# Optimization experiments

Hardware: AMD Instinct MI355X
Metric: run time of the kernel (lower is better)

Reference implementation:

```python
import jax, jax.numpy as jnp
import numpy as np

N = 100000

def _gcn_norm(edge_index, n):
    row, col = edge_index[0], edge_index[1]
    deg = jnp.zeros((n,), jnp.float32).at[col].add(1.0)
    dinv = jnp.where(deg > 0, jax.lax.rsqrt(jnp.maximum(deg, 1.0)), 0.0)
    return dinv[row] * dinv[col]


def _arma_conv(x, row, col, norm, init_w, w, root_w, bias):
    # x: [N, Fin]; init_w: [K, Fin, F]; w: [T-1, K, F, F]; root_w: [T, K, Fin, F]; bias: [T, K, 1, F]
    out = jnp.einsum('nf,kfg->kng', x, init_w)  # [K, N, F]
    T = root_w.shape[0]
    for t in range(T):
        if t > 0:
            out = jnp.einsum('kng,kgh->knh', out, w[t - 1])
        msg = out[:, row, :] * norm[None, :, None]          # [K, E, F] gather
        out = jnp.zeros_like(out).at[:, col, :].add(msg)    # scatter-add to targets
        out = out + jnp.einsum('nf,kfg->kng', x, root_w[t]) + bias[t]
        out = jax.nn.relu(out)
    return out.mean(axis=0)  # average over stacks K


def setup_inputs() -> dict:
    key = jax.random.key(0)
    ks = jax.random.split(key, 12)
    E, Fin, H, C, K = 1600000, 128, 64, 41, 2
    s = 0.1
    return {
        'x': jax.random.normal(ks[0], (N, Fin), jnp.float32),
        'edge_index': jax.random.randint(ks[1], (2, E), 0, N, jnp.int64),
        'w1_init': jax.random.normal(ks[2], (K, Fin, H), jnp.float32) * s,
        'w1': jax.random.normal(ks[3], (1, K, H, H), jnp.float32) * s,
        'w1_root': jax.random.normal(ks[4], (2, K, Fin, H), jnp.float32) * s,
        'b1': jax.random.normal(ks[5], (2, K, 1, H), jnp.float32) * s,
        'w2_init': jax.random.normal(ks[6], (K, H, C), jnp.float32) * s,
        'w2': jax.random.normal(ks[7], (1, K, C, C), jnp.float32) * s,
        'w2_root': jax.random.normal(ks[8], (2, K, H, C), jnp.float32) * s,
        'b2': jax.random.normal(ks[9], (2, K, 1, C), jnp.float32) * s,
    }


def reference(x, edge_index, w1_init, w1, w1_root, b1, w2_init, w2, w2_root, b2):
    row, col = edge_index[0], edge_index[1]
    norm = _gcn_norm(edge_index, N)
    h = jax.nn.relu(_arma_conv(x, row, col, norm, w1_init, w1, w1_root, b1))
    # F.dropout is identity in eval mode
    h = _arma_conv(h, row, col, norm, w2_init, w2, w2_root, b2)
    return jax.nn.log_softmax(h, axis=1)
```

## Files before the change

### kernel.cpp

```cpp
#include <hip/hip_runtime.h>
#include <math.h>

#define TPB 256
typedef unsigned short ushort_t;
typedef unsigned int uint_t;
typedef __attribute__((ext_vector_type(8))) short bf16x8;
typedef __attribute__((ext_vector_type(4))) float f32x4;

__device__ __forceinline__ float bf2f(ushort_t h) {
    return __uint_as_float(((uint_t)h) << 16);
}
__device__ __forceinline__ ushort_t f2bf(float f) {
    uint_t u = __float_as_uint(f);
    u += 0x7fff + ((u >> 16) & 1);
    return (ushort_t)(u >> 16);
}
__device__ __forceinline__ uint_t pack2(float x, float y) {
    return (uint_t)f2bf(x) | ((uint_t)f2bf(y) << 16);
}

__global__ void rank_kernel(const int* __restrict__ col, int* __restrict__ cnt,
                            unsigned short* __restrict__ pos, int E) {
    int e = blockIdx.x * blockDim.x + threadIdx.x;
    if (e < E) pos[e] = (unsigned short)atomicAdd(&cnt[col[e]], 1);
}

__global__ void scan_block(const int* __restrict__ cnt, int* __restrict__ incl,
                           int* __restrict__ bsum, int N) {
    __shared__ int s[TPB];
    int i = blockIdx.x * TPB + threadIdx.x;
    s[threadIdx.x] = (i < N) ? ((cnt[i] + 3) & ~3) : 0;
    __syncthreads();
    for (int d = 1; d < TPB; d <<= 1) {
        int t = (threadIdx.x >= d) ? s[threadIdx.x - d] : 0;
        __syncthreads();
        s[threadIdx.x] += t;
        __syncthreads();
    }
    if (i < N) incl[i] = s[threadIdx.x];
    if (threadIdx.x == TPB - 1) bsum[blockIdx.x] = s[TPB - 1];
}

__global__ void scan_bsums(int* __restrict__ bsum, int nb) {
    __shared__ int s[512];
    int t = threadIdx.x;
    int v = (t < nb) ? bsum[t] : 0;
    s[t] = v;
    __syncthreads();
    for (int d = 1; d < 512; d <<= 1) {
        int u = (t >= d) ? s[t - d] : 0;
        __syncthreads();
        s[t] += u;
        __syncthreads();
    }
    if (t < nb) bsum[t] = s[t] - v;
}

__global__ void finalize_csr(const int* __restrict__ incl, const int* __restrict__ bsum,
                             const int* __restrict__ cnt, int* __restrict__ rowstart,
                             float* __restrict__ dinv, int N) {
    int i = blockIdx.x * TPB + threadIdx.x;
    if (i < N) {
        rowstart[i + 1] = incl[i] + bsum[blockIdx.x];
        int d = cnt[i];
        dinv[i] = (d > 0) ? rsqrtf((float)d) : 0.0f;
    }
    if (i == 0) rowstart[0] = 0;
}

__global__ void fill_csr(const int* __restrict__ row, const int* __restrict__ col,
                         const int* __restrict__ rowstart, const unsigned short* __restrict__ pos,
                         int* __restrict__ srcidx, int E) {
    int e = blockIdx.x * blockDim.x + threadIdx.x;
    if (e < E) srcidx[rowstart[col[e]] + (int)pos[e]] = row[e];
}

__global__ void pad_csr(const int* __restrict__ rowstart, const int* __restrict__ cnt,
                        int* __restrict__ srcidx, int N) {
    int i = blockIdx.x * blockDim.x + threadIdx.x;
    if (i >= N) return;
    int b = rowstart[i] + cnt[i], en = rowstart[i + 1];
    for (int e = b; e < en; ++e) srcidx[e] = N;
}

__global__ void cvt4_kernel(const float4* __restrict__ src, uint2* __restrict__ dst, int n4) {
    int i = blockIdx.x * blockDim.x + threadIdx.x;
    if (i < n4) {
        float4 v = src[i];
        dst[i] = make_uint2(pack2(v.x, v.y), pack2(v.z, v.w));
    }
}

#define SWZ_A 32768
#define SWZ_B 24576
#define SWZ_C 12288
#define SWZ_D 12288
__global__ void swz_all(const float* __restrict__ w1_init, const float* __restrict__ w1,
                        const float* __restrict__ w1_root, const float* __restrict__ w2_init,
                        const float* __restrict__ w2, const float* __restrict__ w2_root,
                        short* __restrict__ dst) {
    int idx = blockIdx.x * blockDim.x + threadIdx.x;
    int region, base, CH, CT;
    if (idx < SWZ_A)                          { region = 0; base = 0; CH = 4; CT = 8; }
    else if (idx < SWZ_A + SWZ_B)             { region = 1; base = SWZ_A; CH = 6; CT = 4; }
    else if (idx < SWZ_A + SWZ_B + SWZ_C)     { region = 2; base = SWZ_A + SWZ_B; CH = 2; CT = 6; }
    else if (idx < SWZ_A + SWZ_B + SWZ_C + SWZ_D)
                                              { region = 3; base = SWZ_A + SWZ_B + SWZ_C; CH = 4; CT = 3; }
    else return;
    int r = idx - base;
    int j = r & 7, ln = (r >> 3) & 63;
    int rest = r >> 9;
    int ct = rest % CT, c = (rest / CT) % CH, k = rest / (CT * CH);
    int col = ct * 16 + (ln & 15);
    int kl = (ln >> 4) * 8 + j;
    float v = 0.0f;
    if (region == 0) {
        int kk = c * 32 + kl;
        if (col < 64)       v = w1_init[((size_t)k * 128 + kk) * 64 + col];
        else                v = w1_root[((size_t)k * 128 + kk) * 64 + (col - 64)];
    } else if (region == 1) {
        if (c < 2) { int kk = c * 32 + kl;        v = w1[((size_t)k * 64 + kk) * 64 + col]; }
        else       { int kk = (c - 2) * 32 + kl;  v = w1_root[((size_t)(2 + k) * 128 + kk) * 64 + col]; }
    } else if (region == 2) {
        int kk = c * 32 + kl;
        if (col < 48) { if (col < 41)            v = w2_init[((size_t)k * 64 + kk) * 41 + col]; }
        else          { int c2 = col - 48; if (c2 < 41) v = w2_root[((size_t)k * 64 + kk) * 41 + c2]; }
    } else {
        if (c < 2) { int kk = c * 32 + kl;       if (kk < 41 && col < 41) v = w2[((size_t)k * 41 + kk) * 41 + col]; }
        else       { int kk = (c - 2) * 32 + kl; if (col < 41)            v = w2_root[((size_t)(2 + k) * 64 + kk) * 41 + col]; }
    }
    dst[(size_t)base + r] = (short)f2bf(v);
}

template<int CT, int CTA, int CH>
__global__ __launch_bounds__(256, 4)
void gemm_t0(const ushort_t* __restrict__ s2, int s2s, const short* __restrict__ fragbuf,
             const float* __restrict__ biasB, const float* __restrict__ dinv,
             int FB, int N, uint_t* __restrict__ pre, uint_t* __restrict__ outH) {
    constexpr int PP = (CT - CTA) * 8;
    constexpr int PA = CTA * 8;
    const int k = blockIdx.y;
    const int n0 = blockIdx.x * 128;
    const int t = threadIdx.x;
    const int w = t >> 6, lane = t & 63, quad = lane >> 4, lr = lane & 15;
    const short* fb = fragbuf + (size_t)k * CH * CT * 512;

    int r0 = n0 + w * 32 + lr;
    int m0 = r0 < N ? r0 : N - 1;
    int m1 = (r0 + 16) < N ? (r0 + 16) : N - 1;

    bf16x8 a0v[CH], a1v[CH];
#pragma unroll
    for (int c = 0; c < CH; ++c) {
        int off = c * 32 + quad * 8;
        a0v[c] = *(const bf16x8*)&s2[(size_t)m0 * s2s + off];
        a1v[c] = *(const bf16x8*)&s2[(size_t)m1 * s2s + off];
    }

    __shared__ short lds_b[CH * CT * 512];
    {
        constexpr int CHUNKS = CH * CT * 64;
#pragma unroll
        for (int i = 0; i < (CHUNKS + 255) / 256; ++i) {
            int idx = i * 256 + t;
            if (CHUNKS % 256 == 0 || idx < CHUNKS)
                *(bf16x8*)&lds_b[idx * 8] = *(const bf16x8*)&fb[(size_t)idx * 8];
        }
    }
    __syncthreads();

    f32x4 acc[2][CT];
#pragma unroll
    for (int rt = 0; rt < 2; ++rt)
#pragma unroll
        for (int ct = 0; ct < CT; ++ct) acc[rt][ct] = (f32x4){0.f, 0.f, 0.f, 0.f};

#pragma unroll
    for (int c = 0; c < CH; ++c) {
#pragma unroll
        for (int ct = 0; ct < CT; ++ct) {
            bf16x8 b = *(const bf16x8*)&lds_b[((size_t)c * CT + ct) * 512 + lane * 8];
            acc[0][ct] = __builtin_amdgcn_mfma_f32_16x16x32_bf16(a0v[c], b, acc[0][ct], 0, 0, 0);
            acc[1][ct] = __builtin_amdgcn_mfma_f32_16x16x32_bf16(a1v[c], b, acc[1][ct], 0, 0, 0);
        }
    }

#pragma unroll
    for (int rt = 0; rt < 2; ++rt) {
#pragma unroll
        for (int i = 0; i < 4; ++i) {
            int n = n0 + w * 32 + rt * 16 + quad * 4 + i;
            if (n >= N) continue;
            float dnv = dinv[n];
#pragma unroll
            for (int ct = 0; ct < CT; ++ct) {
                int col = ct * 16 + lr;
                float v = acc[rt][ct][i];
                if (ct < CTA) {
                    v *= dnv;
                } else {
                    int c2 = col - CTA * 16;
                    if (c2 < FB) v += biasB[(size_t)k * FB + c2];
                }
                float vn = __shfl_xor(v, 1);
                uint_t p = pack2(v, vn);
                uint_t p2 = __shfl_xor(p, 2);
                if (!(lr & 3)) {
                    if (ct < CTA) {
                        *(uint2*)&outH[((size_t)n * 2 + k) * PA + (col >> 1)] = make_uint2(p, p2);
                    } else {
                        int c2 = col - CTA * 16;
                        *(uint2*)&pre[((size_t)n * 2 + k) * PP + (c2 >> 1)] = make_uint2(p, p2);
                    }
                }
            }
        }
    }
}

__global__ __launch_bounds__(256, 3)
void gemm_t1_l1(const ushort_t* __restrict__ s1, const ushort_t* __restrict__ xh,
                const short* __restrict__ fragbuf, const float* __restrict__ bias,
                int N, uint_t* __restrict__ hhU) {
    constexpr int CT = 4, CH = 6;
    const int n0 = blockIdx.x * 128;
    const int t = threadIdx.x;
    const int w = t >> 6, lane = t & 63, quad = lane >> 4, lr = lane & 15;

    int r0 = n0 + w * 32 + lr;
    int m0 = r0 < N ? r0 : N - 1;
    int m1 = (r0 + 16) < N ? (r0 + 16) : N - 1;

    bf16x8 s0a[2][2], s1a[2][2];
    bf16x8 x0a[4], x1a[4];
#pragma unroll
    for (int c = 0; c < 2; ++c) {
        int off = c * 32 + quad * 8;
#pragma unroll
        for (int kk = 0; kk < 2; ++kk) {
            s0a[c][kk] = *(const bf16x8*)&s1[((size_t)m0 * 2 + kk) * 64 + off];
            s1a[c][kk] = *(const bf16x8*)&s1[((size_t)m1 * 2 + kk) * 64 + off];
        }
    }
#pragma unroll
    for (int c = 0; c < 4; ++c) {
        int off = c * 32 + quad * 8;
        x0a[c] = *(const bf16x8*)&xh[(size_t)m0 * 128 + off];
        x1a[c] = *(const bf16x8*)&xh[(size_t)m1 * 128 + off];
    }

    __shared__ short lds_b[2 * CH * CT * 512];
    {
        constexpr int CHUNKS = 2 * CH * CT * 64;
#pragma unroll
        for (int i = 0; i < CHUNKS / 256; ++i) {
            int idx = i * 256 + t;
            *(bf16x8*)&lds_b[idx * 8] = *(const bf16x8*)&fragbuf[(size_t)idx * 8];
        }
    }
    __syncthreads();

    f32x4 acc[2][2][CT];
#pragma unroll
    for (int k = 0; k < 2; ++k)
#pragma unroll
        for (int rt = 0; rt < 2; ++rt)
#pragma unroll
            for (int ct = 0; ct < CT; ++ct) acc[k][rt][ct] = (f32x4){0.f, 0.f, 0.f, 0.f};

#pragma unroll
    for (int c = 0; c < CH; ++c) {
#pragma unroll
        for (int k = 0; k < 2; ++k) {
            bf16x8 a0 = (c < 2) ? s0a[c][k] : x0a[c - 2];
            bf16x8 a1 = (c < 2) ? s1a[c][k] : x1a[c - 2];
#pragma unroll
            for (int ct = 0; ct < CT; ++ct) {
                bf16x8 b = *(const bf16x8*)&lds_b[(((size_t)k * CH + c) * CT + ct) * 512 + lane * 8];
                acc[k][0][ct] = __builtin_amdgcn_mfma_f32_16x16x32_bf16(a0, b, acc[k][0][ct], 0, 0, 0);
                acc[k][1][ct] = __builtin_amdgcn_mfma_f32_16x16x32_bf16(a1, b, acc[k][1][ct], 0, 0, 0);
            }
        }
    }

#pragma unroll
    for (int rt = 0; rt < 2; ++rt) {
#pragma unroll
        for (int i = 0; i < 4; ++i) {
            int n = n0 + w * 32 + rt * 16 + quad * 4 + i;
            if (n >= N) continue;
#pragma unroll
            for (int ct = 0; ct < CT; ++ct) {
                int col = ct * 16 + lr;
                float v0 = fmaxf(acc[0][rt][ct][i] + bias[col], 0.0f);
                float v1 = fmaxf(acc[1][rt][ct][i] + bias[64 + col], 0.0f);
                float m = 0.5f * (v0 + v1);
                float mn = __shfl_xor(m, 1);
                uint_t p = pack2(m, mn);
                uint_t p2 = __shfl_xor(p, 2);
                if (!(lr & 3)) *(uint2*)&hhU[(size_t)n * 32 + (col >> 1)] = make_uint2(p, p2);
            }
        }
    }
}

__global__ __launch_bounds__(256, 3)
void gemm_t1_l2(const ushort_t* __restrict__ s1, const ushort_t* __restrict__ hh,
                const short* __restrict__ fragbuf, const float* __restrict__ bias,
                int N, float* __restrict__ out) {
    constexpr int CT = 3, CH = 4;
    const int n0 = blockIdx.x * 128;
    const int t = threadIdx.x;
    const int w = t >> 6, lane = t & 63, quad = lane >> 4, lr = lane & 15;

    int r0 = n0 + w * 32 + lr;
    int m0 = r0 < N ? r0 : N - 1;
    int m1 = (r0 + 16) < N ? (r0 + 16) : N - 1;

    bf16x8 s0a[2][2], s1a[2][2];
    bf16x8 h0a[2], h1a[2];
#pragma unroll
    for (int c = 0; c < 2; ++c) {
        int off = c * 32 + quad * 8;
#pragma unroll
        for (int kk = 0; kk < 2; ++kk) {
            s0a[c][kk] = *(const bf16x8*)&s1[((size_t)m0 * 2 + kk) * 48 + off];
            s1a[c][kk] = *(const bf16x8*)&s1[((size_t)m1 * 2 + kk) * 48 + off];
        }
    }
#pragma unroll
    for (int c = 0; c < 2; ++c) {
        int off = c * 32 + quad * 8;
        h0a[c] = *(const bf16x8*)&hh[(size_t)m0 * 64 + off];
        h1a[c] = *(const bf16x8*)&hh[(size_t)m1 * 64 + off];
    }

    __shared__ short lds_b[2 * CH * CT * 512];
    {
        constexpr int CHUNKS = 2 * CH * CT * 64;
#pragma unroll
        for (int i = 0; i < CHUNKS / 256; ++i) {
            int idx = i * 256 + t;
            *(bf16x8*)&lds_b[idx * 8] = *(const bf16x8*)&fragbuf[(size_t)idx * 8];
        }
    }
    __syncthreads();

    f32x4 acc[2][2][CT];
#pragma unroll
    for (int k = 0; k < 2; ++k)
#pragma unroll
        for (int rt = 0; rt < 2; ++rt)
#pragma unroll
            for (int ct = 0; ct < CT; ++ct) acc[k][rt][ct] = (f32x4){0.f, 0.f, 0.f, 0.f};

#pragma unroll
    for (int c = 0; c < CH; ++c) {
#pragma unroll
        for (int k = 0; k < 2; ++k) {
            bf16x8 a0 = (c < 2) ? s0a[c][k] : h0a[c - 2];
            bf16x8 a1 = (c < 2) ? s1a[c][k] : h1a[c - 2];
#pragma unroll
            for (int ct = 0; ct < CT; ++ct) {
                bf16x8 b = *(const bf16x8*)&lds_b[(((size_t)k * CH + c) * CT + ct) * 512 + lane * 8];
                acc[k][0][ct] = __builtin_amdgcn_mfma_f32_16x16x32_bf16(a0, b, acc[k][0][ct], 0, 0, 0);
                acc[k][1][ct] = __builtin_amdgcn_mfma_f32_16x16x32_bf16(a1, b, acc[k][1][ct], 0, 0, 0);
            }
        }
    }

#pragma unroll
    for (int rt = 0; rt < 2; ++rt) {
#pragma unroll
        for (int i = 0; i < 4; ++i) {
            int n = n0 + w * 32 + rt * 16 + quad * 4 + i;
            float m[CT];
            float mx = -1e30f;
#pragma unroll
            for (int ct = 0; ct < CT; ++ct) {
                int col = ct * 16 + lr;
                float b0 = (col < 41) ? bias[col] : 0.0f;
                float b1v = (col < 41) ? bias[41 + col] : 0.0f;
                float v0 = fmaxf(acc[0][rt][ct][i] + b0, 0.0f);
                float v1 = fmaxf(acc[1][rt][ct][i] + b1v, 0.0f);
                m[ct] = 0.5f * (v0 + v1);
                if (col < 41) mx = fmaxf(mx, m[ct]);
            }
#pragma unroll
            for (int msk = 1; msk < 16; msk <<= 1) mx = fmaxf(mx, __shfl_xor(mx, msk));
            float s = 0.0f;
#pragma unroll
            for (int ct = 0; ct < CT; ++ct) {
                int col = ct * 16 + lr;
                if (col < 41) s += __expf(m[ct] - mx);
            }
#pragma unroll
            for (int msk = 1; msk < 16; msk <<= 1) s += __shfl_xor(s, msk);
            float ls = __logf(s);
            if (n < N) {
#pragma unroll
                for (int ct = 0; ct < CT; ++ct) {
                    int col = ct * 16 + lr;
                    if (col < 41) out[(size_t)n * 41 + col] = m[ct] - mx - ls;
                }
            }
        }
    }
}

template<int PAIRS, bool SCALE_OUT>
__global__ __launch_bounds__(256)
void gather(const int* __restrict__ rowstart, const int* __restrict__ srcidx,
            const float* __restrict__ dinv, const uint_t* __restrict__ msg,
            const uint_t* __restrict__ pre, uint_t* __restrict__ outH, int N) {
    int gt = blockIdx.x * 256 + threadIdx.x;
    int n = gt >> 6, lane = gt & 63;
    if (n >= N) return;
    int k, pair;
    if (PAIRS == 32) { k = lane >> 5; pair = lane & 31; }
    else { k = lane / PAIRS; pair = lane - k * PAIRS; }
    if (k >= 2) return;
    const int STR = 2 * PAIRS;
    const uint_t lo = (uint_t)(k * PAIRS + pair);
    int beg = rowstart[n], end = rowstart[n + 1];
    float dn = dinv[n];
    size_t o = (size_t)n * STR + lo;
    uint_t p = 0;
    if (pre) p = pre[o];

    float ax0 = 0.f, ax1 = 0.f, ay0 = 0.f, ay1 = 0.f;
    int e = beg;
    for (; e + 8 <= end; e += 8) {
        int4 sa = *(const int4*)&srcidx[e];
        int4 sb = *(const int4*)&srcidx[e + 4];
        uint_t m0 = msg[(uint_t)(sa.x * STR) + lo];
        uint_t m1 = msg[(uint_t)(sa.y * STR) + lo];
        uint_t m2 = msg[(uint_t)(sa.z * STR) + lo];
        uint_t m3 = msg[(uint_t)(sa.w * STR) + lo];
        uint_t m4 = msg[(uint_t)(sb.x * STR) + lo];
        uint_t m5 = msg[(uint_t)(sb.y * STR) + lo];
        uint_t m6 = msg[(uint_t)(sb.z * STR) + lo];
        uint_t m7 = msg[(uint_t)(sb.w * STR) + lo];
        ax0 += __uint_as_float(m0 << 16); ay0 += __uint_as_float(m0 & 0xffff0000u);
        ax1 += __uint_as_float(m1 << 16); ay1 += __uint_as_float(m1 & 0xffff0000u);
        ax0 += __uint_as_float(m2 << 16); ay0 += __uint_as_float(m2 & 0xffff0000u);
        ax1 += __uint_as_float(m3 << 16); ay1 += __uint_as_float(m3 & 0xffff0000u);
        ax0 += __uint_as_float(m4 << 16); ay0 += __uint_as_float(m4 & 0xffff0000u);
        ax1 += __uint_as_float(m5 << 16); ay1 += __uint_as_float(m5 & 0xffff0000u);
        ax0 += __uint_as_float(m6 << 16); ay0 += __uint_as_float(m6 & 0xffff0000u);
        ax1 += __uint_as_float(m7 << 16); ay1 += __uint_as_float(m7 & 0xffff0000u);
    }
    if (e < end) {
        int4 sa = *(const int4*)&srcidx[e];
        uint_t m0 = msg[(uint_t)(sa.x * STR) + lo];
        uint_t m1 = msg[(uint_t)(sa.y * STR) + lo];
        uint_t m2 = msg[(uint_t)(sa.z * STR) + lo];
        uint_t m3 = msg[(uint_t)(sa.w * STR) + lo];
        ax0 += __uint_as_float(m0 << 16); ay0 += __uint_as_float(m0 & 0xffff0000u);
        ax1 += __uint_as_float(m1 << 16); ay1 += __uint_as_float(m1 & 0xffff0000u);
        ax0 += __uint_as_float(m2 << 16); ay0 += __uint_as_float(m2 & 0xffff0000u);
        ax1 += __uint_as_float(m3 << 16); ay1 += __uint_as_float(m3 & 0xffff0000u);
    }
    float ax = (ax0 + ax1) * dn;
    float ay = (ay0 + ay1) * dn;
    if (pre) {
        ax = fmaxf(ax + bf2f((ushort_t)p), 0.0f);
        ay = fmaxf(ay + bf2f((ushort_t)(p >> 16)), 0.0f);
    }
    if (SCALE_OUT) { ax *= dn; ay *= dn; }
    outH[o] = pack2(ax, ay);
}

extern "C" void kernel_launch(void* const* d_in, const int* in_sizes, int n_in,
                              void* d_out, int out_size, void* d_ws, size_t ws_size,
                              hipStream_t stream) {
    const float* x       = (const float*)d_in[0];
    const int*   ei      = (const int*)  d_in[1];
    const float* w1_init = (const float*)d_in[2];
    const float* w1      = (const float*)d_in[3];
    const float* w1_root = (const float*)d_in[4];
    const float* b1      = (const float*)d_in[5];
    const float* w2_init = (const float*)d_in[6];
    const float* w2      = (const float*)d_in[7];
    const float* w2_root = (const float*)d_in[8];
    const float* b2      = (const float*)d_in[9];

    const int Fin1 = 128;
    int N = in_sizes[0] / Fin1;
    int E = in_sizes[1] / 2;
    const int* row = ei;
    const int* col = ei + E;

    char* ws = (char*)d_ws;
    size_t off = 0;
    auto carve = [&](size_t bytes) -> void* {
        void* p = ws + off;
        off += (bytes + 255) & ~(size_t)255;
        return p;
    };
    int nblkN = (N + TPB - 1) / TPB;
    int*      cnt      = (int*)     carve((size_t)N * 4);
    int*      incl     = (int*)     carve((size_t)N * 4);
    int*      rowstart = (int*)     carve((size_t)(N + 1) * 4);
    int*      bsum     = (int*)     carve((size_t)nblkN * 4);
    float*    dinv     = (float*)   carve((size_t)N * 4);
    unsigned short* pos = (unsigned short*)carve((size_t)E * 2);
    int*      srcidx   = (int*)     carve((size_t)(E + 3 * (size_t)N + 64) * 4);
    short*    swz      = (short*)   carve((size_t)(SWZ_A + SWZ_B + SWZ_C + SWZ_D) * 2);
    ushort_t* xh       = (ushort_t*)carve((size_t)N * 128 * 2);
    ushort_t* hh       = (ushort_t*)carve((size_t)N * 64 * 2);
    ushort_t* b16A     = (ushort_t*)carve((size_t)N * 2 * 64 * 2 + 256);
    ushort_t* b16B     = (ushort_t*)carve((size_t)N * 2 * 64 * 2 + 256);
    uint_t*   pre      = (uint_t*)  carve((size_t)N * 2 * 32 * 4);

    hipMemsetAsync((char*)b16A + (size_t)N * 256, 0, 256, stream);
    hipMemsetAsync((char*)b16B + (size_t)N * 256, 0, 256, stream);

    hipMemsetAsync(cnt, 0, (size_t)N * 4, stream);
    rank_kernel <<<(E + TPB - 1) / TPB, TPB, 0, stream>>>(col, cnt, pos, E);
    scan_block  <<<nblkN, TPB, 0, stream>>>(cnt, incl, bsum, N);
    scan_bsums  <<<1, 512, 0, stream>>>(bsum, nblkN);
    finalize_csr<<<nblkN, TPB, 0, stream>>>(incl, bsum, cnt, rowstart, dinv, N);
    pad_csr     <<<nblkN, TPB, 0, stream>>>(rowstart, cnt, srcidx, N);
    fill_csr    <<<(E + TPB - 1) / TPB, TPB, 0, stream>>>(row, col, rowstart, pos, srcidx, E);

    int swztot = SWZ_A + SWZ_B + SWZ_C + SWZ_D;
    swz_all<<<(swztot + TPB - 1) / TPB, TPB, 0, stream>>>(w1_init, w1, w1_root,
                                                          w2_init, w2, w2_root, swz);
    int nx4 = N * 128 / 4;
    cvt4_kernel<<<(nx4 + TPB - 1) / TPB, TPB, 0, stream>>>((const float4*)x, (uint2*)xh, nx4);

    dim3 gg2((N + 127) / 128, 2);
    dim3 gg1((N + 127) / 128, 1);
    int ggb = (N * 64 + TPB - 1) / TPB;
    const short* swzA = swz;
    const short* swzB = swz + SWZ_A;
    const short* swzC = swz + SWZ_A + SWZ_B;
    const short* swzD = swz + SWZ_A + SWZ_B + SWZ_C;

    gemm_t0<8, 4, 4><<<gg2, TPB, 0, stream>>>(xh, 128, swzA, b1, dinv, 64, N, pre, (uint_t*)b16A);
    gather<32, true ><<<ggb, TPB, 0, stream>>>(rowstart, srcidx, dinv, (const uint_t*)b16A,
                                               pre, (uint_t*)b16B, N);
    gather<32, false><<<ggb, TPB, 0, stream>>>(rowstart, srcidx, dinv, (const uint_t*)b16B,
                                               nullptr, (uint_t*)b16A, N);
    gemm_t1_l1<<<gg1, TPB, 0, stream>>>(b16A, xh, swzB, b1 + 2 * 64, N, (uint_t*)hh);

    hipMemsetAsync((char*)b16A + (size_t)N * 192, 0, 192, stream);
    hipMemsetAsync((char*)b16B + (size_t)N * 192, 0, 192, stream);

    gemm_t0<6, 3, 2><<<gg2, TPB, 0, stream>>>(hh, 64, swzC, b2, dinv, 41, N, pre, (uint_t*)b16A);
    gather<24, true ><<<ggb, TPB, 0, stream>>>(rowstart, srcidx, dinv, (const uint_t*)b16A,
                                               pre, (uint_t*)b16B, N);
    gather<24, false><<<ggb, TPB, 0, stream>>>(rowstart, srcidx, dinv, (const uint_t*)b16B,
                                               nullptr, (uint_t*)b16A, N);
    gemm_t1_l2<<<gg1, TPB, 0, stream>>>(b16A, hh, swzD, b2 + 2 * 41, N, (float*)d_out);
}
```

Baseline: 563.0 us.

## Fuse preprocessing kernels, overlap CSR fill with first GEMM, tighten layer-2 gather

Merges the edge-rank, weight-swizzle and x-to-bf16 conversion into one launch, since those three steps are independent. Folds the CSR fill and pad work into extra blocks of the first GEMM, interleaved so both run concurrently. Specialises the layer-2 gather to use 48 threads per node instead of 64, which removes idle lanes. This cuts launch count and tail idle time, but the fused GEMM grid now has mixed block types that may hurt occupancy or LDS scheduling.

Result: slower. 592.2 us (+5.2%).

```diff
diff --git a/kernel.cpp b/kernel.cpp
--- a/kernel.cpp
+++ b/kernel.cpp
@@ -19,10 +19,64 @@
     return (uint_t)f2bf(x) | ((uint_t)f2bf(y) << 16);
 }
 
-__global__ void rank_kernel(const int* __restrict__ col, int* __restrict__ cnt,
-                            unsigned short* __restrict__ pos, int E) {
-    int e = blockIdx.x * blockDim.x + threadIdx.x;
-    if (e < E) pos[e] = (unsigned short)atomicAdd(&cnt[col[e]], 1);
+#define SWZ_A 32768
+#define SWZ_B 24576
+#define SWZ_C 12288
+#define SWZ_D 12288
+
+__global__ __launch_bounds__(256)
+void pre1(const int* __restrict__ col, int* __restrict__ cnt, unsigned short* __restrict__ pos,
+          int E, int nEb,
+          const float* __restrict__ w1_init, const float* __restrict__ w1,
+          const float* __restrict__ w1_root, const float* __restrict__ w2_init,
+          const float* __restrict__ w2, const float* __restrict__ w2_root,
+          short* __restrict__ swzdst, int nSb,
+          const float4* __restrict__ x, uint2* __restrict__ xh, int n4) {
+    int b = blockIdx.x;
+    if (b < nEb) {
+        int e = b * 256 + threadIdx.x;
+        if (e < E) pos[e] = (unsigned short)atomicAdd(&cnt[col[e]], 1);
+        return;
+    }
+    if (b < nEb + nSb) {
+        int idx = (b - nEb) * 256 + threadIdx.x;
+        int region, base, CH, CT;
+        if (idx < SWZ_A)                          { region = 0; base = 0; CH = 4; CT = 8; }
+        else if (idx < SWZ_A + SWZ_B)             { region = 1; base = SWZ_A; CH = 6; CT = 4; }
+        else if (idx < SWZ_A + SWZ_B + SWZ_C)     { region = 2; base = SWZ_A + SWZ_B; CH = 2; CT = 6; }
+        else if (idx < SWZ_A + SWZ_B + SWZ_C + SWZ_D)
+                                                  { region = 3; base = SWZ_A + SWZ_B + SWZ_C; CH = 4; CT = 3; }
+        else return;
+        int r = idx - base;
+        int j = r & 7, ln = (r >> 3) & 63;
+        int rest = r >> 9;
+        int ct = rest % CT, c = (rest / CT) % CH, k = rest / (CT * CH);
+        int colm = ct * 16 + (ln & 15);
+        int kl = (ln >> 4) * 8 + j;
+        float v = 0.0f;
+        if (region == 0) {
+            int kk = c * 32 + kl;
+            if (colm < 64)       v = w1_init[((size_t)k * 128 + kk) * 64 + colm];
+            else                 v = w1_root[((size_t)k * 128 + kk) * 64 + (colm - 64)];
+        } else if (region == 1) {
+            if (c < 2) { int kk = c * 32 + kl;        v = w1[((size_t)k * 64 + kk) * 64 + colm]; }
+            else       { int kk = (c - 2) * 32 + kl;  v = w1_root[((size_t)(2 + k) * 128 + kk) * 64 + colm]; }
+        } else if (region == 2) {
+            int kk = c * 32 + kl;
+            if (colm < 48) { if (colm < 41)           v = w2_init[((size_t)k * 64 + kk) * 41 + colm]; }
+            else           { int c2 = colm - 48; if (c2 < 41) v = w2_root[((size_t)k * 64 + kk) * 41 + c2]; }
+        } else {
+            if (c < 2) { int kk = c * 32 + kl;       if (kk < 41 && colm < 41) v = w2[((size_t)k * 41 + kk) * 41 + colm]; }
+            else       { int kk = (c - 2) * 32 + kl; if (colm < 41)            v = w2_root[((size_t)(2 + k) * 64 + kk) * 41 + colm]; }
+        }
+        swzdst[(size_t)base + r] = (short)f2bf(v);
+        return;
+    }
+    int i = (b - nEb - nSb) * 256 + threadIdx.x;
+    if (i < n4) {
+        float4 v = x[i];
+        xh[i] = make_uint2(pack2(v.x, v.y), pack2(v.z, v.w));
+    }
 }
 
 __global__ void scan_block(const int* __restrict__ cnt, int* __restrict__ incl,
@@ -68,79 +122,47 @@
     if (i == 0) rowstart[0] = 0;
 }
 
-__global__ void fill_csr(const int* __restrict__ row, const int* __restrict__ col,
-                         const int* __restrict__ rowstart, const unsigned short* __restrict__ pos,
-                         int* __restrict__ srcidx, int E) {
-    int e = blockIdx.x * blockDim.x + threadIdx.x;
-    if (e < E) srcidx[rowstart[col[e]] + (int)pos[e]] = row[e];
-}
-
-__global__ void pad_csr(const int* __restrict__ rowstart, const int* __restrict__ cnt,
-                        int* __restrict__ srcidx, int N) {
-    int i = blockIdx.x * blockDim.x + threadIdx.x;
-    if (i >= N) return;
-    int b = rowstart[i] + cnt[i], en = rowstart[i + 1];
-    for (int e = b; e < en; ++e) srcidx[e] = N;
-}
-
-__global__ void cvt4_kernel(const float4* __restrict__ src, uint2* __restrict__ dst, int n4) {
-    int i = blockIdx.x * blockDim.x + threadIdx.x;
-    if (i < n4) {
-        float4 v = src[i];
-        dst[i] = make_uint2(pack2(v.x, v.y), pack2(v.z, v.w));
-    }
-}
-
-#define SWZ_A 32768
-#define SWZ_B 24576
-#define SWZ_C 12288
-#define SWZ_D 12288
-__global__ void swz_all(const float* __restrict__ w1_init, const float* __restrict__ w1,
-                        const float* __restrict__ w1_root, const float* __restrict__ w2_init,
-                        const float* __restrict__ w2, const float* __restrict__ w2_root,
-                        short* __restrict__ dst) {
-    int idx = blockIdx.x * blockDim.x + threadIdx.x;
-    int region, base, CH, CT;
-    if (idx < SWZ_A)                          { region = 0; base = 0; CH = 4; CT = 8; }
-    else if (idx < SWZ_A + SWZ_B)             { region = 1; base = SWZ_A; CH = 6; CT = 4; }
-    else if (idx < SWZ_A + SWZ_B + SWZ_C)     { region = 2; base = SWZ_A + SWZ_B; CH = 2; CT = 6; }
-    else if (idx < SWZ_A + SWZ_B + SWZ_C + SWZ_D)
-                                              { region = 3; base = SWZ_A + SWZ_B + SWZ_C; CH = 4; CT = 3; }
-    else return;
-    int r = idx - base;
-    int j = r & 7, ln = (r >> 3) & 63;
-    int rest = r >> 9;
-    int ct = rest % CT, c = (rest / CT) % CH, k = rest / (CT * CH);
-    int col = ct * 16 + (ln & 15);
-    int kl = (ln >> 4) * 8 + j;
-    float v = 0.0f;
-    if (region == 0) {
-        int kk = c * 32 + kl;
-        if (col < 64)       v = w1_init[((size_t)k * 128 + kk) * 64 + col];
-        else                v = w1_root[((size_t)k * 128 + kk) * 64 + (col - 64)];
-    } else if (region == 1) {
-        if (c < 2) { int kk = c * 32 + kl;        v = w1[((size_t)k * 64 + kk) * 64 + col]; }
-        else       { int kk = (c - 2) * 32 + kl;  v = w1_root[((size_t)(2 + k) * 128 + kk) * 64 + col]; }
-    } else if (region == 2) {
-        int kk = c * 32 + kl;
-        if (col < 48) { if (col < 41)            v = w2_init[((size_t)k * 64 + kk) * 41 + col]; }
-        else          { int c2 = col - 48; if (c2 < 41) v = w2_root[((size_t)k * 64 + kk) * 41 + c2]; }
-    } else {
-        if (c < 2) { int kk = c * 32 + kl;       if (kk < 41 && col < 41) v = w2[((size_t)k * 41 + kk) * 41 + col]; }
-        else       { int kk = (c - 2) * 32 + kl; if (col < 41)            v = w2_root[((size_t)(2 + k) * 64 + kk) * 41 + col]; }
-    }
-    dst[(size_t)base + r] = (short)f2bf(v);
-}
-
 template<int CT, int CTA, int CH>
 __global__ __launch_bounds__(256, 4)
-void gemm_t0(const ushort_t* __restrict__ s2, int s2s, const short* __restrict__ fragbuf,
-             const float* __restrict__ biasB, const float* __restrict__ dinv,
-             int FB, int N, uint_t* __restrict__ pre, uint_t* __restrict__ outH) {
+void gemm_t0_f(const ushort_t* __restrict__ s2, int s2s, const short* __restrict__ fragbuf,
+               const float* __restrict__ biasB, const float* __restrict__ dinv,
+               int FB, int N, uint_t* __restrict__ pre, uint_t* __restrict__ outH,
+               int GB, int fbBlocks,
+               const int* __restrict__ rowv, const int* __restrict__ colv,
+               const int* __restrict__ rowstart, const unsigned short* __restrict__ pos,
+               const int* __restrict__ cnt, int* __restrict__ srcidx, int E) {
     constexpr int PP = (CT - CTA) * 8;
     constexpr int PA = CTA * 8;
-    const int k = blockIdx.y;
-    const int n0 = blockIdx.x * 128;
+    __shared__ short lds_b[CH * CT * 512];
+
+    int gid;
+    {
+        int b = blockIdx.x;
+        if (fbBlocks == 0) {
+            gid = b;
+        } else {
+            int r = b & 7, c = b >> 3;
+            if (r < 2) {
+                gid = c * 2 + r;
+            } else {
+                int fid = c * 6 + (r - 2);
+                if (fid < fbBlocks) {
+                    int id = fid * 256 + (int)threadIdx.x;
+                    if (id < E) {
+                        srcidx[rowstart[colv[id]] + (int)pos[id]] = rowv[id];
+                    } else if (id - E < N) {
+                        int i = id - E;
+                        int bg = rowstart[i] + cnt[i], en = rowstart[i + 1];
+                        for (int e = bg; e < en; ++e) srcidx[e] = N;
+                    }
+                }
+                return;
+            }
+        }
+    }
+    if (gid >= GB * 2) return;
+    const int k = gid / GB;
+    const int n0 = (gid - k * GB) * 128;
     const int t = threadIdx.x;
     const int w = t >> 6, lane = t & 63, quad = lane >> 4, lr = lane & 15;
     const short* fb = fragbuf + (size_t)k * CH * CT * 512;
@@ -157,7 +179,6 @@
         a1v[c] = *(const bf16x8*)&s2[(size_t)m1 * s2s + off];
     }
 
-    __shared__ short lds_b[CH * CT * 512];
     {
         constexpr int CHUNKS = CH * CT * 64;
 #pragma unroll
@@ -179,9 +200,9 @@
     for (int c = 0; c < CH; ++c) {
 #pragma unroll
         for (int ct = 0; ct < CT; ++ct) {
-            bf16x8 b = *(const bf16x8*)&lds_b[((size_t)c * CT + ct) * 512 + lane * 8];
-            acc[0][ct] = __builtin_amdgcn_mfma_f32_16x16x32_bf16(a0v[c], b, acc[0][ct], 0, 0, 0);
-            acc[1][ct] = __builtin_amdgcn_mfma_f32_16x16x32_bf16(a1v[c], b, acc[1][ct], 0, 0, 0);
+            bf16x8 bfr = *(const bf16x8*)&lds_b[((size_t)c * CT + ct) * 512 + lane * 8];
+            acc[0][ct] = __builtin_amdgcn_mfma_f32_16x16x32_bf16(a0v[c], bfr, acc[0][ct], 0, 0, 0);
+            acc[1][ct] = __builtin_amdgcn_mfma_f32_16x16x32_bf16(a1v[c], bfr, acc[1][ct], 0, 0, 0);
         }
     }
 
@@ -408,20 +429,16 @@
     }
 }
 
-template<int PAIRS, bool SCALE_OUT>
+template<bool SCALE_OUT>
 __global__ __launch_bounds__(256)
-void gather(const int* __restrict__ rowstart, const int* __restrict__ srcidx,
-            const float* __restrict__ dinv, const uint_t* __restrict__ msg,
-            const uint_t* __restrict__ pre, uint_t* __restrict__ outH, int N) {
+void gather32(const int* __restrict__ rowstart, const int* __restrict__ srcidx,
+              const float* __restrict__ dinv, const uint_t* __restrict__ msg,
+              const uint_t* __restrict__ pre, uint_t* __restrict__ outH, int N) {
     int gt = blockIdx.x * 256 + threadIdx.x;
-    int n = gt >> 6, lane = gt & 63;
+    int n = gt >> 6;
     if (n >= N) return;
-    int k, pair;
-    if (PAIRS == 32) { k = lane >> 5; pair = lane & 31; }
-    else { k = lane / PAIRS; pair = lane - k * PAIRS; }
-    if (k >= 2) return;
-    const int STR = 2 * PAIRS;
-    const uint_t lo = (uint_t)(k * PAIRS + pair);
+    const uint_t lo = (uint_t)(gt & 63);
+    const int STR = 64;
     int beg = rowstart[n], end = rowstart[n + 1];
     float dn = dinv[n];
     size_t o = (size_t)n * STR + lo;
@@ -471,6 +488,65 @@
     outH[o] = pack2(ax, ay);
 }
 
+template<bool SCALE_OUT>
+__global__ __launch_bounds__(256)
+void gather24(const int* __restrict__ rowstart, const int* __restrict__ srcidx,
+              const float* __restrict__ dinv, const uint_t* __restrict__ msg,
+              const uint_t* __restrict__ pre, uint_t* __restrict__ outH, int N) {
+    int gt = blockIdx.x * 256 + threadIdx.x;
+    int n = gt / 48;
+    if (n >= N) return;
+    const uint_t lo = (uint_t)(gt - n * 48);
+    const int STR = 48;
+    int beg = rowstart[n], end = rowstart[n + 1];
+    float dn = dinv[n];
+    size_t o = (size_t)n * STR + lo;
+    uint_t p = 0;
+    if (pre) p = pre[o];
+
+    float ax0 = 0.f, ax1 = 0.f, ay0 = 0.f, ay1 = 0.f;
+    int e = beg;
+    for (; e + 8 <= end; e += 8) {
+        int4 sa = *(const int4*)&srcidx[e];
+        int4 sb = *(const int4*)&srcidx[e + 4];
+        uint_t m0 = msg[(uint_t)(sa.x * STR) + lo];
+        uint_t m1 = msg[(uint_t)(sa.y * STR) + lo];
+        uint_t m2 = msg[(uint_t)(sa.z * STR) + lo];
+        uint_t m3 = msg[(uint_t)(sa.w * STR) + lo];
+        uint_t m4 = msg[(uint_t)(sb.x * STR) + lo];
+        uint_t m5 = msg[(uint_t)(sb.y * STR) + lo];
+        uint_t m6 = msg[(uint_t)(sb.z * STR) + lo];
+        uint_t m7 = msg[(uint_t)(sb.w * STR) + lo];
+        ax0 += __uint_as_float(m0 << 16); ay0 += __uint_as_float(m0 & 0xffff0000u);
+        ax1 += __uint_as_float(m1 << 16); ay1 += __uint_as_float(m1 & 0xffff0000u);
+        ax0 += __uint_as_float(m2 << 16); ay0 += __uint_as_float(m2 & 0xffff0000u);
+        ax1 += __uint_as_float(m3 << 16); ay1 += __uint_as_float(m3 & 0xffff0000u);
+        ax0 += __uint_as_float(m4 << 16); ay0 += __uint_as_float(m4 & 0xffff0000u);
+        ax1 += __uint_as_float(m5 << 16); ay1 += __uint_as_float(m5 & 0xffff0000u);
+        ax0 += __uint_as_float(m6 << 16); ay0 += __uint_as_float(m6 & 0xffff0000u);
+        ax1 += __uint_as_float(m7 << 16); ay1 += __uint_as_float(m7 & 0xffff0000u);
+    }
+    if (e < end) {
+        int4 sa = *(const int4*)&srcidx[e];
+        uint_t m0 = msg[(uint_t)(sa.x * STR) + lo];
+        uint_t m1 = msg[(uint_t)(sa.y * STR) + lo];
+        uint_t m2 = msg[(uint_t)(sa.z * STR) + lo];
+        uint_t m3 = msg[(uint_t)(sa.w * STR) + lo];
+        ax0 += __uint_as_float(m0 << 16); ay0 += __uint_as_float(m0 & 0xffff0000u);
+        ax1 += __uint_as_float(m1 << 16); ay1 += __uint_as_float(m1 & 0xffff0000u);
+        ax0 += __uint_as_float(m2 << 16); ay0 += __uint_as_float(m2 & 0xffff0000u);
+        ax1 += __uint_as_float(m3 << 16); ay1 += __uint_as_float(m3 & 0xffff0000u);
+    }
+    float ax = (ax0 + ax1) * dn;
+    float ay = (ay0 + ay1) * dn;
+    if (pre) {
+        ax = fmaxf(ax + bf2f((ushort_t)p), 0.0f);
+        ay = fmaxf(ay + bf2f((ushort_t)(p >> 16)), 0.0f);
+    }
+    if (SCALE_OUT) { ax *= dn; ay *= dn; }
+    outH[o] = pack2(ax, ay);
+}
+
 extern "C" void kernel_launch(void* const* d_in, const int* in_sizes, int n_in,
                               void* d_out, int out_size, void* d_ws, size_t ws_size,
                               hipStream_t stream) {
@@ -515,43 +591,51 @@
 
     hipMemsetAsync((char*)b16A + (size_t)N * 256, 0, 256, stream);
     hipMemsetAsync((char*)b16B + (size_t)N * 256, 0, 256, stream);
-
     hipMemsetAsync(cnt, 0, (size_t)N * 4, stream);
-    rank_kernel <<<(E + TPB - 1) / TPB, TPB, 0, stream>>>(col, cnt, pos, E);
+
+    int nEb = (E + TPB - 1) / TPB;
+    int swztot = SWZ_A + SWZ_B + SWZ_C + SWZ_D;
+    int nSb = (swztot + TPB - 1) / TPB;
+    int n4 = N * 128 / 4;
+    int nCb = (n4 + TPB - 1) / TPB;
+    pre1<<<nEb + nSb + nCb, TPB, 0, stream>>>(col, cnt, pos, E, nEb,
+                                              w1_init, w1, w1_root, w2_init, w2, w2_root,
+                                              swz, nSb, (const float4*)x, (uint2*)xh, n4);
+
     scan_block  <<<nblkN, TPB, 0, stream>>>(cnt, incl, bsum, N);
     scan_bsums  <<<1, 512, 0, stream>>>(bsum, nblkN);
     finalize_csr<<<nblkN, TPB, 0, stream>>>(incl, bsum, cnt, rowstart, dinv, N);
-    pad_csr     <<<nblkN, TPB, 0, stream>>>(rowstart, cnt, srcidx, N);
-    fill_csr    <<<(E + TPB - 1) / TPB, TPB, 0, stream>>>(row, col, rowstart, pos, srcidx, E);
-
-    int swztot = SWZ_A + SWZ_B + SWZ_C + SWZ_D;
-    swz_all<<<(swztot + TPB - 1) / TPB, TPB, 0, stream>>>(w1_init, w1, w1_root,
-                                                          w2_init, w2, w2_root, swz);
-    int nx4 = N * 128 / 4;
-    cvt4_kernel<<<(nx4 + TPB - 1) / TPB, TPB, 0, stream>>>((const float4*)x, (uint2*)xh, nx4);
-
-    dim3 gg2((N + 127) / 128, 2);
-    dim3 gg1((N + 127) / 128, 1);
-    int ggb = (N * 64 + TPB - 1) / TPB;
+
     const short* swzA = swz;
     const short* swzB = swz + SWZ_A;
     const short* swzC = swz + SWZ_A + SWZ_B;
     const short* swzD = swz + SWZ_A + SWZ_B + SWZ_C;
-
-    gemm_t0<8, 4, 4><<<gg2, TPB, 0, stream>>>(xh, 128, swzA, b1, dinv, 64, N, pre, (uint_t*)b16A);
-    gather<32, true ><<<ggb, TPB, 0, stream>>>(rowstart, srcidx, dinv, (const uint_t*)b16A,
-                                               pre, (uint_t*)b16B, N);
-    gather<32, false><<<ggb, TPB, 0, stream>>>(rowstart, srcidx, dinv, (const uint_t*)b16B,
-                                               nullptr, (uint_t*)b16A, N);
+    dim3 gg1((N + 127) / 128, 1);
+    int GB = (N + 127) / 128;
+    int g32 = (N * 64 + TPB - 1) / TPB;
+    int g24 = (N * 48 + TPB - 1) / TPB;
+
+    int FBb = (E + N + TPB - 1) / TPB;
+    int C1 = max((GB * 2 + 1) / 2, (FBb + 5) / 6);
+    gemm_t0_f<8, 4, 4><<<C1 * 8, TPB, 0, stream>>>(xh, 128, swzA, b1, dinv, 64, N,
+                                                   pre, (uint_t*)b16A, GB, FBb,
+                                                   row, col, rowstart, pos, cnt, srcidx, E);
+
+    gather32<true ><<<g32, TPB, 0, stream>>>(rowstart, srcidx, dinv, (const uint_t*)b16A,
+                                             pre, (uint_t*)b16B, N);
+    gather32<false><<<g32, TPB, 0, stream>>>(rowstart, srcidx, dinv, (const uint_t*)b16B,
+                                             nullptr, (uint_t*)b16A, N);
     gemm_t1_l1<<<gg1, TPB, 0, stream>>>(b16A, xh, swzB, b1 + 2 * 64, N, (uint_t*)hh);
 
     hipMemsetAsync((char*)b16A + (size_t)N * 192, 0, 192, stream);
     hipMemsetAsync((char*)b16B + (size_t)N * 192, 0, 192, stream);
 
-    gemm_t0<6, 3, 2><<<gg2, TPB, 0, stream>>>(hh, 64, swzC, b2, dinv, 41, N, pre, (uint_t*)b16A);
-    gather<24, true ><<<ggb, TPB, 0, stream>>>(rowstart, srcidx, dinv, (const uint_t*)b16A,
-                                               pre, (uint_t*)b16B, N);
-    gather<24, false><<<ggb, TPB, 0, stream>>>(rowstart, srcidx, dinv, (const uint_t*)b16B,
-                                               nullptr, (uint_t*)b16A, N);
+    gemm_t0_f<6, 3, 2><<<GB * 2, TPB, 0, stream>>>(hh, 64, swzC, b2, dinv, 41, N,
+                                                   pre, (uint_t*)b16A, GB, 0,
+                                                   nullptr, nullptr, nullptr, nullptr, nullptr, nullptr, 0);
+    gather24<true ><<<g24, TPB, 0, stream>>>(rowstart, srcidx, dinv, (const uint_t*)b16A,
+                                             pre, (uint_t*)b16B, N);
+    gather24<false><<<g24, TPB, 0, stream>>>(rowstart, srcidx, dinv, (const uint_t*)b16B,
+                                             nullptr, (uint_t*)b16A, N);
     gemm_t1_l2<<<gg1, TPB, 0, stream>>>(b16A, hh, swzD, b2 + 2 * 41, N, (float*)d_out);
 }
```
